# Performance work log

Measured on AMD Instinct MI355X. Metric: run time of the kernel, lower is better.

The kernel has to match this reference:

```python
import jax, jax.numpy as jnp
import numpy as np

U, I, D = 100000, 150000, 64
N = U + I
E = 1250000
KEEP_RATE = 0.8


def setup_inputs() -> dict:
    key = jax.random.key(0)
    k1, k2, k3, k4, k5, k6 = jax.random.split(key, 6)
    row = jax.random.randint(k1, (E,), 0, N, dtype=jnp.int32)
    col = jax.random.randint(k2, (E,), 0, N, dtype=jnp.int32)
    adj_values = jax.random.uniform(k3, (E,), dtype=jnp.float32)
    # edge dropout mask: floor(rand + keep_rate) in {0,1}, exactly as SpAdjEdgeDrop
    edge_mask = jnp.floor(jax.random.uniform(k4, (E,), dtype=jnp.float32) + KEEP_RATE)
    user_embeds = jax.random.normal(k5, (U, D), dtype=jnp.float32)
    item_embeds = jax.random.normal(k6, (I, D), dtype=jnp.float32)
    return {
        "row": row,
        "col": col,
        "adj_values": adj_values,
        "edge_mask": edge_mask,
        "user_embeds": user_embeds,
        "item_embeds": item_embeds,
        "layer_num": 3,
    }


def reference(row, col, adj_values, edge_mask, user_embeds, item_embeds, layer_num):
    user_num = user_embeds.shape[0]
    n_nodes = user_num + item_embeds.shape[0]
    # edge-dropped sparse values (mask==0 edges contribute nothing to spmm)
    vals = adj_values * edge_mask  # [E]
    embeds = jnp.concatenate([user_embeds, item_embeds], axis=0)  # [N, D]
    acc = embeds
    cur = embeds
    for _ in range(layer_num):
        # spmm: out[r] += vals[e] * cur[c] for each edge e=(r,c)
        msgs = vals[:, None] * cur[col]  # [E, D] gather
        cur = jax.ops.segment_sum(msgs, row, num_segments=n_nodes)  # [N, D] scatter-add
        acc = acc + cur
    out = acc / (layer_num + 1)
    return out[:user_num], out[user_num:]
```

## Files before the change

### kernel.cpp

```cpp
#include <hip/hip_runtime.h>


#define U_NODES 100000
#define N_NODES 250000
#define DIM4 16
#define E_EDGES 1250000
#define TILE_ROWS 1024
#define NT 245
#define NB 1024
#define GSZ (NB * 256)
#define BSEG 1280

typedef unsigned short u16;

__device__ __forceinline__ float bf2f(u16 h) {
    return __uint_as_float(((unsigned)h) << 16);
}
__device__ __forceinline__ u16 f2bf(float f) {
    unsigned u = __float_as_uint(f);
    u += 0x7fffu + ((u >> 16) & 1u);
    return (u16)(u >> 16);
}
__device__ __forceinline__ ushort4 gat(const u16* __restrict__ base, int node, int part) {
    return ((const ushort4*)(base + ((size_t)node << 6)))[part];
}
__device__ __forceinline__ void fma4(float4& s, float v, ushort4 h) {
    s.x += v * bf2f(h.x);
    s.y += v * bf2f(h.y);
    s.z += v * bf2f(h.z);
    s.w += v * bf2f(h.w);
}

__global__ void lgcn_part(const float4* __restrict__ user4,
                          const float4* __restrict__ item4,
                          u16* __restrict__ e0b,
                          const int* __restrict__ row,
                          const int* __restrict__ col,
                          const float* __restrict__ adj,
                          const float* __restrict__ mask,
                          int* __restrict__ OFF,
                          int2* __restrict__ staging) {
    __shared__ int lhist[256];
    __shared__ int lscan[256];
    __shared__ int loff[256];
    __shared__ int lcur[256];
    const int t = threadIdx.x;
    const int b = blockIdx.x;
    const int g0 = b * 256 + t;

    lhist[t] = 0;
    __syncthreads();

    for (int e = g0; e < E_EDGES; e += GSZ)
        if (mask[e] != 0.0f) atomicAdd(&lhist[row[e] >> 10], 1);
    __syncthreads();

    int v = lhist[t];
    lscan[t] = v;
    __syncthreads();
    for (int off = 1; off < 256; off <<= 1) {
        int u = (t >= off) ? lscan[t - off] : 0;
        __syncthreads();
        if (t >= off) lscan[t] += u;
        __syncthreads();
    }
    loff[t] = lscan[t] - v;
    lcur[t] = 0;
    __syncthreads();

    OFF[b * 256 + t] = loff[t];

    for (int e = g0; e < E_EDGES; e += GSZ) {
        float m = mask[e];
        if (m == 0.0f) continue;
        int r = row[e];
        int bkt = r >> 10;
        int rank = loff[bkt] + atomicAdd(&lcur[bkt], 1);
        staging[(size_t)b * BSEG + rank] =
            make_int2(((r & 1023) << 18) | col[e], __float_as_int(adj[e] * m));
    }

    const int CONV = N_NODES * 8;
    for (int i = g0; i < CONV; i += GSZ) {
        const int uc = U_NODES * 8;
        const float4* src = (i < uc) ? (user4 + 2 * (long)i)
                                     : (item4 + 2 * (long)(i - uc));
        float4 a = src[0];
        float4 bb = src[1];
        int4 o;
        o.x = (int)((unsigned)f2bf(a.x) | ((unsigned)f2bf(a.y) << 16));
        o.y = (int)((unsigned)f2bf(a.z) | ((unsigned)f2bf(a.w) << 16));
        o.z = (int)((unsigned)f2bf(bb.x) | ((unsigned)f2bf(bb.y) << 16));
        o.w = (int)((unsigned)f2bf(bb.z) | ((unsigned)f2bf(bb.w) << 16));
        ((int4*)e0b)[i] = o;
    }
}

__global__ void lgcn_build(const int* __restrict__ OFF,
                           const int2* __restrict__ staging,
                           int* __restrict__ total,
                           int2* __restrict__ rowdesc,
                           int2* __restrict__ csr) {
    __shared__ int S[NB];
    __shared__ int boff[NB];
    __shared__ int lcount[TILE_ROWS];
    __shared__ int lstart[TILE_ROWS];
    __shared__ int lcur[TILE_ROWS];
    __shared__ int lscan[256];
    __shared__ int sbase;
    const int i = blockIdx.x;
    const int t = threadIdx.x;

    int o0 = OFF[(4 * t + 0) * 256 + i], e0 = OFF[(4 * t + 0) * 256 + i + 1];
    int o1 = OFF[(4 * t + 1) * 256 + i], e1 = OFF[(4 * t + 1) * 256 + i + 1];
    int o2 = OFF[(4 * t + 2) * 256 + i], e2 = OFF[(4 * t + 2) * 256 + i + 1];
    int o3 = OFF[(4 * t + 3) * 256 + i], e3 = OFF[(4 * t + 3) * 256 + i + 1];
    int c0 = e0 - o0, c1 = e1 - o1, c2 = e2 - o2, c3 = e3 - o3;
    boff[4 * t + 0] = o0; boff[4 * t + 1] = o1;
    boff[4 * t + 2] = o2; boff[4 * t + 3] = o3;
    int sl = c0 + c1 + c2 + c3;
    lscan[t] = sl;
    __syncthreads();
    for (int off = 1; off < 256; off <<= 1) {
        int u = (t >= off) ? lscan[t - off] : 0;
        __syncthreads();
        if (t >= off) lscan[t] += u;
        __syncthreads();
    }
    int ex = lscan[t] - sl;
    S[4 * t + 0] = ex;
    S[4 * t + 1] = ex + c0;
    S[4 * t + 2] = ex + c0 + c1;
    S[4 * t + 3] = ex + c0 + c1 + c2;
    const int T = lscan[255];
    lcount[t] = 0; lcount[t + 256] = 0; lcount[t + 512] = 0; lcount[t + 768] = 0;
    __syncthreads();

    for (int j = t; j < T; j += 256) {
        int lo = 0, hi = NB;
        while (hi - lo > 1) { int mid = (lo + hi) >> 1; if (S[mid] <= j) lo = mid; else hi = mid; }
        int2 rec = staging[(size_t)lo * BSEG + boff[lo] + (j - S[lo])];
        atomicAdd(&lcount[((unsigned)rec.x) >> 18], 1);
    }
    __syncthreads();

    int d0 = lcount[4 * t + 0], d1 = lcount[4 * t + 1];
    int d2 = lcount[4 * t + 2], d3 = lcount[4 * t + 3];
    int p0 = (d0 + 3) & ~3, p1 = (d1 + 3) & ~3, p2 = (d2 + 3) & ~3, p3 = (d3 + 3) & ~3;
    int s = p0 + p1 + p2 + p3;
    __syncthreads();
    lscan[t] = s;
    __syncthreads();
    for (int off = 1; off < 256; off <<= 1) {
        int u = (t >= off) ? lscan[t - off] : 0;
        __syncthreads();
        if (t >= off) lscan[t] += u;
        __syncthreads();
    }
    if (t == 255) sbase = atomicAdd(total, lscan[255]);
    __syncthreads();
    const int tilesum = lscan[255];
    int pos = sbase + lscan[t] - s;
    int rbase = i * TILE_ROWS + 4 * t;
    if (rbase + 0 < N_NODES) rowdesc[rbase + 0] = make_int2(pos, d0);
    lstart[4 * t + 0] = pos; lcur[4 * t + 0] = 0; pos += p0;
    if (rbase + 1 < N_NODES) rowdesc[rbase + 1] = make_int2(pos, d1);
    lstart[4 * t + 1] = pos; lcur[4 * t + 1] = 0; pos += p1;
    if (rbase + 2 < N_NODES) rowdesc[rbase + 2] = make_int2(pos, d2);
    lstart[4 * t + 2] = pos; lcur[4 * t + 2] = 0; pos += p2;
    if (rbase + 3 < N_NODES) rowdesc[rbase + 3] = make_int2(pos, d3);
    lstart[4 * t + 3] = pos; lcur[4 * t + 3] = 0;
    __syncthreads();

    for (int j = t; j < tilesum; j += 256) csr[sbase + j] = make_int2(0, 0);
    __syncthreads();

    for (int j = t; j < T; j += 256) {
        int lo = 0, hi = NB;
        while (hi - lo > 1) { int mid = (lo + hi) >> 1; if (S[mid] <= j) lo = mid; else hi = mid; }
        int2 rec = staging[(size_t)lo * BSEG + boff[lo] + (j - S[lo])];
        int rw = ((unsigned)rec.x) >> 18;
        int rank = atomicAdd(&lcur[rw], 1);
        csr[lstart[rw] + rank] = make_int2(rec.x & 0x3FFFF, rec.y);
    }
}

template <bool LAST>
__global__ void lgcn_pull(const int2* __restrict__ rowdesc,
                          const int2* __restrict__ csr,
                          const u16*  __restrict__ curb,
                          const u16*  __restrict__ e0b,
                          const u16*  __restrict__ e1b,
                          u16*        __restrict__ outb,
                          float4*     __restrict__ out) {
    int tid = blockIdx.x * blockDim.x + threadIdx.x;
    int r = tid >> 4;
    int part = tid & 15;
    if (r >= N_NODES) return;
    int2 rd = rowdesc[r];
    int start = rd.x;
    int pend  = start + ((rd.y + 3) & ~3);
    float4 s = make_float4(0.f, 0.f, 0.f, 0.f);
    int e = start;
    for (; e + 8 <= pend; e += 8) {
        int4 ca = *(const int4*)(csr + e);
        int4 cb = *(const int4*)(csr + e + 2);
        int4 cc = *(const int4*)(csr + e + 4);
        int4 cd = *(const int4*)(csr + e + 6);
        ushort4 h0 = gat(curb, ca.x, part);
        ushort4 h1 = gat(curb, ca.z, part);
        ushort4 h2 = gat(curb, cb.x, part);
        ushort4 h3 = gat(curb, cb.z, part);
        ushort4 h4 = gat(curb, cc.x, part);
        ushort4 h5 = gat(curb, cc.z, part);
        ushort4 h6 = gat(curb, cd.x, part);
        ushort4 h7 = gat(curb, cd.z, part);
        fma4(s, __int_as_float(ca.y), h0);
        fma4(s, __int_as_float(ca.w), h1);
        fma4(s, __int_as_float(cb.y), h2);
        fma4(s, __int_as_float(cb.w), h3);
        fma4(s, __int_as_float(cc.y), h4);
        fma4(s, __int_as_float(cc.w), h5);
        fma4(s, __int_as_float(cd.y), h6);
        fma4(s, __int_as_float(cd.w), h7);
    }
    if (e < pend) {
        int4 ca = *(const int4*)(csr + e);
        int4 cb = *(const int4*)(csr + e + 2);
        ushort4 h0 = gat(curb, ca.x, part);
        ushort4 h1 = gat(curb, ca.z, part);
        ushort4 h2 = gat(curb, cb.x, part);
        ushort4 h3 = gat(curb, cb.z, part);
        fma4(s, __int_as_float(ca.y), h0);
        fma4(s, __int_as_float(ca.w), h1);
        fma4(s, __int_as_float(cb.y), h2);
        fma4(s, __int_as_float(cb.w), h3);
    }
    size_t oi = (size_t)r * DIM4 + part;
    if (LAST) {
        ushort4 a0 = ((const ushort4*)e0b)[oi];
        ushort4 a1 = ((const ushort4*)e1b)[oi];
        ushort4 a2 = ((const ushort4*)curb)[oi];
        out[oi] = make_float4(
            (s.x + bf2f(a0.x) + bf2f(a1.x) + bf2f(a2.x)) * 0.25f,
            (s.y + bf2f(a0.y) + bf2f(a1.y) + bf2f(a2.y)) * 0.25f,
            (s.z + bf2f(a0.z) + bf2f(a1.z) + bf2f(a2.z)) * 0.25f,
            (s.w + bf2f(a0.w) + bf2f(a1.w) + bf2f(a2.w)) * 0.25f);
    } else {
        ((ushort4*)outb)[oi] = make_ushort4(f2bf(s.x), f2bf(s.y), f2bf(s.z), f2bf(s.w));
    }
}

extern "C" void kernel_launch(void* const* d_in, const int* in_sizes, int n_in,
                              void* d_out, int out_size, void* d_ws, size_t ws_size,
                              hipStream_t stream) {
    const int*   row  = (const int*)d_in[0];
    const int*   col  = (const int*)d_in[1];
    const float* adj  = (const float*)d_in[2];
    const float* mask = (const float*)d_in[3];
    const float4* user4 = (const float4*)d_in[4];
    const float4* item4 = (const float4*)d_in[5];

    float4* acc = (float4*)d_out;

    const size_t bemb_bytes = (size_t)N_NODES * 64 * sizeof(u16);
    char* p = (char*)d_ws;
    u16* e0b = (u16*)p;  p += bemb_bytes;
    u16* e1b = (u16*)p;  p += bemb_bytes;
    u16* e2b = (u16*)p;  p += bemb_bytes;
    int* total = (int*)p;  p += 64;
    int* OFF   = (int*)p;  p += (size_t)NB * 256 * 4;
    int2* staging = (int2*)p;  p += (size_t)NB * BSEG * 8;
    int2* rowdesc = (int2*)p;  p += ((size_t)N_NODES * 8 + 63) & ~63ul;
    int2* csr     = (int2*)p;

    const int BLK = 256;
    const long node_vec4 = (long)N_NODES * DIM4;
    const int  grid_pull = (int)((node_vec4 + BLK - 1) / BLK);

    hipMemsetAsync(total, 0, 64, stream);
    lgcn_part<<<NB, BLK, 0, stream>>>(user4, item4, e0b, row, col, adj, mask,
                                      OFF, staging);
    lgcn_build<<<NT, BLK, 0, stream>>>(OFF, staging, total, rowdesc, csr);

    lgcn_pull<false><<<grid_pull, BLK, 0, stream>>>(rowdesc, csr, e0b, nullptr, nullptr, e1b, nullptr);
    lgcn_pull<false><<<grid_pull, BLK, 0, stream>>>(rowdesc, csr, e1b, nullptr, nullptr, e2b, nullptr);
    lgcn_pull<true ><<<grid_pull, BLK, 0, stream>>>(rowdesc, csr, e2b, e0b, e1b, nullptr, acc);
}
```

Before: 304.0 us.

## Split CSR build into count, scan, and place kernels with per-bucket parallelism

The single build kernel ran 245 blocks, each doing a binary search per edge to locate staging records. It is replaced by three kernels. Count and place use 4x more blocks; each thread walks one contiguous staging run directly with shared-memory atomics, and a separate scan kernel computes row offsets and per-group start positions. CSR zeroing moves to a hipMemsetAsync. This adds two launches, extra DEG/QSTART buffers and a larger memset over the whole CSR region, and edge order within a row may differ from before.

```diff
diff --git a/kernel.cpp b/kernel.cpp
--- a/kernel.cpp
+++ b/kernel.cpp
@@ -96,30 +96,47 @@
     }
 }
 
-__global__ void lgcn_build(const int* __restrict__ OFF,
+__global__ void lgcn_count(const int* __restrict__ OFF,
                            const int2* __restrict__ staging,
-                           int* __restrict__ total,
-                           int2* __restrict__ rowdesc,
-                           int2* __restrict__ csr) {
-    __shared__ int S[NB];
-    __shared__ int boff[NB];
+                           int* __restrict__ DEG) {
     __shared__ int lcount[TILE_ROWS];
-    __shared__ int lstart[TILE_ROWS];
-    __shared__ int lcur[TILE_ROWS];
+    const int i = blockIdx.x >> 2;
+    const int g = blockIdx.x & 3;
+    const int t = threadIdx.x;
+    lcount[t] = 0; lcount[t + 256] = 0; lcount[t + 512] = 0; lcount[t + 768] = 0;
+    __syncthreads();
+    const int b = (g << 8) + t;
+    const int o = OFF[(b << 8) + i];
+    const int n = OFF[(b << 8) + i + 1] - o;
+    const int2* run = staging + (size_t)b * BSEG + o;
+    for (int j = 0; j < n; ++j)
+        atomicAdd(&lcount[((unsigned)run[j].x) >> 18], 1);
+    __syncthreads();
+    const int base = ((i << 2) + g) << 10;
+    DEG[base + t]       = lcount[t];
+    DEG[base + t + 256] = lcount[t + 256];
+    DEG[base + t + 512] = lcount[t + 512];
+    DEG[base + t + 768] = lcount[t + 768];
+}
+
+__global__ void lgcn_scan(const int* __restrict__ DEG,
+                          int* __restrict__ total,
+                          int2* __restrict__ rowdesc,
+                          int* __restrict__ QSTART) {
     __shared__ int lscan[256];
     __shared__ int sbase;
     const int i = blockIdx.x;
     const int t = threadIdx.x;
-
-    int o0 = OFF[(4 * t + 0) * 256 + i], e0 = OFF[(4 * t + 0) * 256 + i + 1];
-    int o1 = OFF[(4 * t + 1) * 256 + i], e1 = OFF[(4 * t + 1) * 256 + i + 1];
-    int o2 = OFF[(4 * t + 2) * 256 + i], e2 = OFF[(4 * t + 2) * 256 + i + 1];
-    int o3 = OFF[(4 * t + 3) * 256 + i], e3 = OFF[(4 * t + 3) * 256 + i + 1];
-    int c0 = e0 - o0, c1 = e1 - o1, c2 = e2 - o2, c3 = e3 - o3;
-    boff[4 * t + 0] = o0; boff[4 * t + 1] = o1;
-    boff[4 * t + 2] = o2; boff[4 * t + 3] = o3;
-    int sl = c0 + c1 + c2 + c3;
-    lscan[t] = sl;
+    const int base = i << 12;
+
+    int a0 = DEG[base + 4*t+0], b0 = DEG[base+1024 + 4*t+0], c0 = DEG[base+2048 + 4*t+0], d0 = DEG[base+3072 + 4*t+0];
+    int a1 = DEG[base + 4*t+1], b1 = DEG[base+1024 + 4*t+1], c1 = DEG[base+2048 + 4*t+1], d1 = DEG[base+3072 + 4*t+1];
+    int a2 = DEG[base + 4*t+2], b2 = DEG[base+1024 + 4*t+2], c2 = DEG[base+2048 + 4*t+2], d2 = DEG[base+3072 + 4*t+2];
+    int a3 = DEG[base + 4*t+3], b3 = DEG[base+1024 + 4*t+3], c3 = DEG[base+2048 + 4*t+3], d3 = DEG[base+3072 + 4*t+3];
+    int deg0 = a0+b0+c0+d0, deg1 = a1+b1+c1+d1, deg2 = a2+b2+c2+d2, deg3 = a3+b3+c3+d3;
+    int p0 = (deg0+3)&~3, p1 = (deg1+3)&~3, p2 = (deg2+3)&~3, p3 = (deg3+3)&~3;
+    int s = p0 + p1 + p2 + p3;
+    lscan[t] = s;
     __syncthreads();
     for (int off = 1; off < 256; off <<= 1) {
         int u = (t >= off) ? lscan[t - off] : 0;
@@ -127,61 +144,60 @@
         if (t >= off) lscan[t] += u;
         __syncthreads();
     }
-    int ex = lscan[t] - sl;
-    S[4 * t + 0] = ex;
-    S[4 * t + 1] = ex + c0;
-    S[4 * t + 2] = ex + c0 + c1;
-    S[4 * t + 3] = ex + c0 + c1 + c2;
-    const int T = lscan[255];
-    lcount[t] = 0; lcount[t + 256] = 0; lcount[t + 512] = 0; lcount[t + 768] = 0;
-    __syncthreads();
-
-    for (int j = t; j < T; j += 256) {
-        int lo = 0, hi = NB;
-        while (hi - lo > 1) { int mid = (lo + hi) >> 1; if (S[mid] <= j) lo = mid; else hi = mid; }
-        int2 rec = staging[(size_t)lo * BSEG + boff[lo] + (j - S[lo])];
-        atomicAdd(&lcount[((unsigned)rec.x) >> 18], 1);
-    }
-    __syncthreads();
-
-    int d0 = lcount[4 * t + 0], d1 = lcount[4 * t + 1];
-    int d2 = lcount[4 * t + 2], d3 = lcount[4 * t + 3];
-    int p0 = (d0 + 3) & ~3, p1 = (d1 + 3) & ~3, p2 = (d2 + 3) & ~3, p3 = (d3 + 3) & ~3;
-    int s = p0 + p1 + p2 + p3;
-    __syncthreads();
-    lscan[t] = s;
-    __syncthreads();
-    for (int off = 1; off < 256; off <<= 1) {
-        int u = (t >= off) ? lscan[t - off] : 0;
-        __syncthreads();
-        if (t >= off) lscan[t] += u;
-        __syncthreads();
-    }
     if (t == 255) sbase = atomicAdd(total, lscan[255]);
     __syncthreads();
-    const int tilesum = lscan[255];
     int pos = sbase + lscan[t] - s;
-    int rbase = i * TILE_ROWS + 4 * t;
-    if (rbase + 0 < N_NODES) rowdesc[rbase + 0] = make_int2(pos, d0);
-    lstart[4 * t + 0] = pos; lcur[4 * t + 0] = 0; pos += p0;
-    if (rbase + 1 < N_NODES) rowdesc[rbase + 1] = make_int2(pos, d1);
-    lstart[4 * t + 1] = pos; lcur[4 * t + 1] = 0; pos += p1;
-    if (rbase + 2 < N_NODES) rowdesc[rbase + 2] = make_int2(pos, d2);
-    lstart[4 * t + 2] = pos; lcur[4 * t + 2] = 0; pos += p2;
-    if (rbase + 3 < N_NODES) rowdesc[rbase + 3] = make_int2(pos, d3);
-    lstart[4 * t + 3] = pos; lcur[4 * t + 3] = 0;
-    __syncthreads();
-
-    for (int j = t; j < tilesum; j += 256) csr[sbase + j] = make_int2(0, 0);
-    __syncthreads();
-
-    for (int j = t; j < T; j += 256) {
-        int lo = 0, hi = NB;
-        while (hi - lo > 1) { int mid = (lo + hi) >> 1; if (S[mid] <= j) lo = mid; else hi = mid; }
-        int2 rec = staging[(size_t)lo * BSEG + boff[lo] + (j - S[lo])];
+    const int rbase = (i << 10) + 4 * t;
+
+    int q = pos;
+    if (rbase + 0 < N_NODES) rowdesc[rbase + 0] = make_int2(pos, deg0);
+    QSTART[base + 4*t+0] = q; q += a0;
+    QSTART[base+1024 + 4*t+0] = q; q += b0;
+    QSTART[base+2048 + 4*t+0] = q; q += c0;
+    QSTART[base+3072 + 4*t+0] = q;
+    pos += p0; q = pos;
+    if (rbase + 1 < N_NODES) rowdesc[rbase + 1] = make_int2(pos, deg1);
+    QSTART[base + 4*t+1] = q; q += a1;
+    QSTART[base+1024 + 4*t+1] = q; q += b1;
+    QSTART[base+2048 + 4*t+1] = q; q += c1;
+    QSTART[base+3072 + 4*t+1] = q;
+    pos += p1; q = pos;
+    if (rbase + 2 < N_NODES) rowdesc[rbase + 2] = make_int2(pos, deg2);
+    QSTART[base + 4*t+2] = q; q += a2;
+    QSTART[base+1024 + 4*t+2] = q; q += b2;
+    QSTART[base+2048 + 4*t+2] = q; q += c2;
+    QSTART[base+3072 + 4*t+2] = q;
+    pos += p2; q = pos;
+    if (rbase + 3 < N_NODES) rowdesc[rbase + 3] = make_int2(pos, deg3);
+    QSTART[base + 4*t+3] = q; q += a3;
+    QSTART[base+1024 + 4*t+3] = q; q += b3;
+    QSTART[base+2048 + 4*t+3] = q; q += c3;
+    QSTART[base+3072 + 4*t+3] = q;
+}
+
+__global__ void lgcn_place(const int* __restrict__ OFF,
+                           const int2* __restrict__ staging,
+                           const int* __restrict__ QSTART,
+                           int2* __restrict__ csr) {
+    __shared__ int lcur[TILE_ROWS];
+    const int i = blockIdx.x >> 2;
+    const int g = blockIdx.x & 3;
+    const int t = threadIdx.x;
+    const int base = ((i << 2) + g) << 10;
+    lcur[t]       = QSTART[base + t];
+    lcur[t + 256] = QSTART[base + t + 256];
+    lcur[t + 512] = QSTART[base + t + 512];
+    lcur[t + 768] = QSTART[base + t + 768];
+    __syncthreads();
+    const int b = (g << 8) + t;
+    const int o = OFF[(b << 8) + i];
+    const int n = OFF[(b << 8) + i + 1] - o;
+    const int2* run = staging + (size_t)b * BSEG + o;
+    for (int j = 0; j < n; ++j) {
+        int2 rec = run[j];
         int rw = ((unsigned)rec.x) >> 18;
-        int rank = atomicAdd(&lcur[rw], 1);
-        csr[lstart[rw] + rank] = make_int2(rec.x & 0x3FFFF, rec.y);
+        int idx = atomicAdd(&lcur[rw], 1);
+        csr[idx] = make_int2(rec.x & 0x3FFFF, rec.y);
     }
 }
 
@@ -270,18 +286,24 @@
     u16* e2b = (u16*)p;  p += bemb_bytes;
     int* total = (int*)p;  p += 64;
     int* OFF   = (int*)p;  p += (size_t)NB * 256 * 4;
+    int* DEG   = (int*)p;  p += (size_t)NT * 4 * 1024 * 4;
+    int* QSTART= (int*)p;  p += (size_t)NT * 4 * 1024 * 4;
     int2* staging = (int2*)p;  p += (size_t)NB * BSEG * 8;
     int2* rowdesc = (int2*)p;  p += ((size_t)N_NODES * 8 + 63) & ~63ul;
     int2* csr     = (int2*)p;
+    const size_t csr_bytes = ((size_t)E_EDGES + 3 * N_NODES) * 8;
 
     const int BLK = 256;
     const long node_vec4 = (long)N_NODES * DIM4;
     const int  grid_pull = (int)((node_vec4 + BLK - 1) / BLK);
 
     hipMemsetAsync(total, 0, 64, stream);
+    hipMemsetAsync(csr, 0, csr_bytes, stream);
     lgcn_part<<<NB, BLK, 0, stream>>>(user4, item4, e0b, row, col, adj, mask,
                                       OFF, staging);
-    lgcn_build<<<NT, BLK, 0, stream>>>(OFF, staging, total, rowdesc, csr);
+    lgcn_count<<<NT * 4, BLK, 0, stream>>>(OFF, staging, DEG);
+    lgcn_scan<<<NT, BLK, 0, stream>>>(DEG, total, rowdesc, QSTART);
+    lgcn_place<<<NT * 4, BLK, 0, stream>>>(OFF, staging, QSTART, csr);
 
     lgcn_pull<false><<<grid_pull, BLK, 0, stream>>>(rowdesc, csr, e0b, nullptr, nullptr, e1b, nullptr);
     lgcn_pull<false><<<grid_pull, BLK, 0, stream>>>(rowdesc, csr, e1b, nullptr, nullptr, e2b, nullptr);
```

New measurement: 299.7 us. About the same (-1.4%).

## Cache edge rows in registers, walk staging runs directly, use fixed per-tile CSR slots

Applied to the files above, without the earlier changes.

The partition kernel now keeps each thread's five edges' row and mask in registers, so the scatter pass does not reload row and mask. The scatter also moves after the bf16 conversion loop, which may help hide the first pass's latency. The build kernel drops the per-element binary search over source blocks: each thread walks its four contiguous staging runs sequentially. The global atomic tile offset is replaced by a fixed per-tile capacity (TCAP=8192), and zeroing CSR padding becomes one memset. This assumes at most five edges per thread and at most 8192 padded edges per tile, and the sequential per-thread runs may be poorly balanced and uncoalesced.

```diff
diff --git a/kernel.cpp b/kernel.cpp
--- a/kernel.cpp
+++ b/kernel.cpp
@@ -10,6 +10,7 @@
 #define NB 1024
 #define GSZ (NB * 256)
 #define BSEG 1280
+#define TCAP 8192
 
 typedef unsigned short u16;
 
@@ -51,8 +52,20 @@
     lhist[t] = 0;
     __syncthreads();
 
-    for (int e = g0; e < E_EDGES; e += GSZ)
-        if (mask[e] != 0.0f) atomicAdd(&lhist[row[e] >> 10], 1);
+    int r0 = -1, r1 = -1, r2 = -1, r3 = -1, r4 = -1;
+    float v0 = 0.f, v1 = 0.f, v2 = 0.f, v3 = 0.f, v4 = 0.f;
+    {
+        int e = g0;
+        if (e < E_EDGES) { float m = mask[e]; if (m != 0.f) { r0 = row[e]; v0 = m; atomicAdd(&lhist[r0 >> 10], 1); } }
+        e += GSZ;
+        if (e < E_EDGES) { float m = mask[e]; if (m != 0.f) { r1 = row[e]; v1 = m; atomicAdd(&lhist[r1 >> 10], 1); } }
+        e += GSZ;
+        if (e < E_EDGES) { float m = mask[e]; if (m != 0.f) { r2 = row[e]; v2 = m; atomicAdd(&lhist[r2 >> 10], 1); } }
+        e += GSZ;
+        if (e < E_EDGES) { float m = mask[e]; if (m != 0.f) { r3 = row[e]; v3 = m; atomicAdd(&lhist[r3 >> 10], 1); } }
+        e += GSZ;
+        if (e < E_EDGES) { float m = mask[e]; if (m != 0.f) { r4 = row[e]; v4 = m; atomicAdd(&lhist[r4 >> 10], 1); } }
+    }
     __syncthreads();
 
     int v = lhist[t];
@@ -69,16 +82,6 @@
     __syncthreads();
 
     OFF[b * 256 + t] = loff[t];
-
-    for (int e = g0; e < E_EDGES; e += GSZ) {
-        float m = mask[e];
-        if (m == 0.0f) continue;
-        int r = row[e];
-        int bkt = r >> 10;
-        int rank = loff[bkt] + atomicAdd(&lcur[bkt], 1);
-        staging[(size_t)b * BSEG + rank] =
-            make_int2(((r & 1023) << 18) | col[e], __float_as_int(adj[e] * m));
-    }
 
     const int CONV = N_NODES * 8;
     for (int i = g0; i < CONV; i += GSZ) {
@@ -94,61 +97,61 @@
         o.w = (int)((unsigned)f2bf(bb.z) | ((unsigned)f2bf(bb.w) << 16));
         ((int4*)e0b)[i] = o;
     }
+    __syncthreads();
+
+    {
+        int e = g0;
+        if (r0 >= 0) { int bkt = r0 >> 10; int rank = loff[bkt] + atomicAdd(&lcur[bkt], 1);
+            staging[(size_t)b * BSEG + rank] = make_int2(((r0 & 1023) << 18) | col[e], __float_as_int(adj[e] * v0)); }
+        e += GSZ;
+        if (r1 >= 0) { int bkt = r1 >> 10; int rank = loff[bkt] + atomicAdd(&lcur[bkt], 1);
+            staging[(size_t)b * BSEG + rank] = make_int2(((r1 & 1023) << 18) | col[e], __float_as_int(adj[e] * v1)); }
+        e += GSZ;
+        if (r2 >= 0) { int bkt = r2 >> 10; int rank = loff[bkt] + atomicAdd(&lcur[bkt], 1);
+            staging[(size_t)b * BSEG + rank] = make_int2(((r2 & 1023) << 18) | col[e], __float_as_int(adj[e] * v2)); }
+        e += GSZ;
+        if (r3 >= 0) { int bkt = r3 >> 10; int rank = loff[bkt] + atomicAdd(&lcur[bkt], 1);
+            staging[(size_t)b * BSEG + rank] = make_int2(((r3 & 1023) << 18) | col[e], __float_as_int(adj[e] * v3)); }
+        e += GSZ;
+        if (r4 >= 0) { int bkt = r4 >> 10; int rank = loff[bkt] + atomicAdd(&lcur[bkt], 1);
+            staging[(size_t)b * BSEG + rank] = make_int2(((r4 & 1023) << 18) | col[e], __float_as_int(adj[e] * v4)); }
+    }
 }
 
 __global__ void lgcn_build(const int* __restrict__ OFF,
                            const int2* __restrict__ staging,
-                           int* __restrict__ total,
                            int2* __restrict__ rowdesc,
                            int2* __restrict__ csr) {
-    __shared__ int S[NB];
-    __shared__ int boff[NB];
     __shared__ int lcount[TILE_ROWS];
     __shared__ int lstart[TILE_ROWS];
     __shared__ int lcur[TILE_ROWS];
     __shared__ int lscan[256];
-    __shared__ int sbase;
     const int i = blockIdx.x;
     const int t = threadIdx.x;
 
-    int o0 = OFF[(4 * t + 0) * 256 + i], e0 = OFF[(4 * t + 0) * 256 + i + 1];
-    int o1 = OFF[(4 * t + 1) * 256 + i], e1 = OFF[(4 * t + 1) * 256 + i + 1];
-    int o2 = OFF[(4 * t + 2) * 256 + i], e2 = OFF[(4 * t + 2) * 256 + i + 1];
-    int o3 = OFF[(4 * t + 3) * 256 + i], e3 = OFF[(4 * t + 3) * 256 + i + 1];
-    int c0 = e0 - o0, c1 = e1 - o1, c2 = e2 - o2, c3 = e3 - o3;
-    boff[4 * t + 0] = o0; boff[4 * t + 1] = o1;
-    boff[4 * t + 2] = o2; boff[4 * t + 3] = o3;
-    int sl = c0 + c1 + c2 + c3;
-    lscan[t] = sl;
-    __syncthreads();
-    for (int off = 1; off < 256; off <<= 1) {
-        int u = (t >= off) ? lscan[t - off] : 0;
-        __syncthreads();
-        if (t >= off) lscan[t] += u;
-        __syncthreads();
-    }
-    int ex = lscan[t] - sl;
-    S[4 * t + 0] = ex;
-    S[4 * t + 1] = ex + c0;
-    S[4 * t + 2] = ex + c0 + c1;
-    S[4 * t + 3] = ex + c0 + c1 + c2;
-    const int T = lscan[255];
     lcount[t] = 0; lcount[t + 256] = 0; lcount[t + 512] = 0; lcount[t + 768] = 0;
     __syncthreads();
 
-    for (int j = t; j < T; j += 256) {
-        int lo = 0, hi = NB;
-        while (hi - lo > 1) { int mid = (lo + hi) >> 1; if (S[mid] <= j) lo = mid; else hi = mid; }
-        int2 rec = staging[(size_t)lo * BSEG + boff[lo] + (j - S[lo])];
-        atomicAdd(&lcount[((unsigned)rec.x) >> 18], 1);
-    }
+    const int b0 = t, b1 = t + 256, b2 = t + 512, b3 = t + 768;
+    const int o0 = OFF[(b0 << 8) + i], n0 = OFF[(b0 << 8) + i + 1] - o0;
+    const int o1 = OFF[(b1 << 8) + i], n1 = OFF[(b1 << 8) + i + 1] - o1;
+    const int o2 = OFF[(b2 << 8) + i], n2 = OFF[(b2 << 8) + i + 1] - o2;
+    const int o3 = OFF[(b3 << 8) + i], n3 = OFF[(b3 << 8) + i + 1] - o3;
+    const int2* run0 = staging + (size_t)b0 * BSEG + o0;
+    const int2* run1 = staging + (size_t)b1 * BSEG + o1;
+    const int2* run2 = staging + (size_t)b2 * BSEG + o2;
+    const int2* run3 = staging + (size_t)b3 * BSEG + o3;
+
+    for (int j = 0; j < n0; ++j) atomicAdd(&lcount[((unsigned)run0[j].x) >> 18], 1);
+    for (int j = 0; j < n1; ++j) atomicAdd(&lcount[((unsigned)run1[j].x) >> 18], 1);
+    for (int j = 0; j < n2; ++j) atomicAdd(&lcount[((unsigned)run2[j].x) >> 18], 1);
+    for (int j = 0; j < n3; ++j) atomicAdd(&lcount[((unsigned)run3[j].x) >> 18], 1);
     __syncthreads();
 
     int d0 = lcount[4 * t + 0], d1 = lcount[4 * t + 1];
     int d2 = lcount[4 * t + 2], d3 = lcount[4 * t + 3];
     int p0 = (d0 + 3) & ~3, p1 = (d1 + 3) & ~3, p2 = (d2 + 3) & ~3, p3 = (d3 + 3) & ~3;
     int s = p0 + p1 + p2 + p3;
-    __syncthreads();
     lscan[t] = s;
     __syncthreads();
     for (int off = 1; off < 256; off <<= 1) {
@@ -157,32 +160,26 @@
         if (t >= off) lscan[t] += u;
         __syncthreads();
     }
-    if (t == 255) sbase = atomicAdd(total, lscan[255]);
-    __syncthreads();
-    const int tilesum = lscan[255];
-    int pos = sbase + lscan[t] - s;
-    int rbase = i * TILE_ROWS + 4 * t;
+    int pos = i * TCAP + lscan[t] - s;
+    const int rbase = (i << 10) + 4 * t;
     if (rbase + 0 < N_NODES) rowdesc[rbase + 0] = make_int2(pos, d0);
-    lstart[4 * t + 0] = pos; lcur[4 * t + 0] = 0; pos += p0;
+    lstart[4 * t + 0] = pos; lcur[4 * t + 0] = pos; pos += p0;
     if (rbase + 1 < N_NODES) rowdesc[rbase + 1] = make_int2(pos, d1);
-    lstart[4 * t + 1] = pos; lcur[4 * t + 1] = 0; pos += p1;
+    lstart[4 * t + 1] = pos; lcur[4 * t + 1] = pos; pos += p1;
     if (rbase + 2 < N_NODES) rowdesc[rbase + 2] = make_int2(pos, d2);
-    lstart[4 * t + 2] = pos; lcur[4 * t + 2] = 0; pos += p2;
+    lstart[4 * t + 2] = pos; lcur[4 * t + 2] = pos; pos += p2;
     if (rbase + 3 < N_NODES) rowdesc[rbase + 3] = make_int2(pos, d3);
-    lstart[4 * t + 3] = pos; lcur[4 * t + 3] = 0;
-    __syncthreads();
-
-    for (int j = t; j < tilesum; j += 256) csr[sbase + j] = make_int2(0, 0);
-    __syncthreads();
-
-    for (int j = t; j < T; j += 256) {
-        int lo = 0, hi = NB;
-        while (hi - lo > 1) { int mid = (lo + hi) >> 1; if (S[mid] <= j) lo = mid; else hi = mid; }
-        int2 rec = staging[(size_t)lo * BSEG + boff[lo] + (j - S[lo])];
-        int rw = ((unsigned)rec.x) >> 18;
-        int rank = atomicAdd(&lcur[rw], 1);
-        csr[lstart[rw] + rank] = make_int2(rec.x & 0x3FFFF, rec.y);
-    }
+    lstart[4 * t + 3] = pos; lcur[4 * t + 3] = pos;
+    __syncthreads();
+
+    for (int j = 0; j < n0; ++j) { int2 rec = run0[j]; int rw = ((unsigned)rec.x) >> 18;
+        csr[atomicAdd(&lcur[rw], 1)] = make_int2(rec.x & 0x3FFFF, rec.y); }
+    for (int j = 0; j < n1; ++j) { int2 rec = run1[j]; int rw = ((unsigned)rec.x) >> 18;
+        csr[atomicAdd(&lcur[rw], 1)] = make_int2(rec.x & 0x3FFFF, rec.y); }
+    for (int j = 0; j < n2; ++j) { int2 rec = run2[j]; int rw = ((unsigned)rec.x) >> 18;
+        csr[atomicAdd(&lcur[rw], 1)] = make_int2(rec.x & 0x3FFFF, rec.y); }
+    for (int j = 0; j < n3; ++j) { int2 rec = run3[j]; int rw = ((unsigned)rec.x) >> 18;
+        csr[atomicAdd(&lcur[rw], 1)] = make_int2(rec.x & 0x3FFFF, rec.y); }
 }
 
 template <bool LAST>
@@ -268,20 +265,20 @@
     u16* e0b = (u16*)p;  p += bemb_bytes;
     u16* e1b = (u16*)p;  p += bemb_bytes;
     u16* e2b = (u16*)p;  p += bemb_bytes;
-    int* total = (int*)p;  p += 64;
     int* OFF   = (int*)p;  p += (size_t)NB * 256 * 4;
     int2* staging = (int2*)p;  p += (size_t)NB * BSEG * 8;
     int2* rowdesc = (int2*)p;  p += ((size_t)N_NODES * 8 + 63) & ~63ul;
     int2* csr     = (int2*)p;
+    const size_t csr_bytes = (size_t)NT * TCAP * 8;
 
     const int BLK = 256;
     const long node_vec4 = (long)N_NODES * DIM4;
     const int  grid_pull = (int)((node_vec4 + BLK - 1) / BLK);
 
-    hipMemsetAsync(total, 0, 64, stream);
+    hipMemsetAsync(csr, 0, csr_bytes, stream);
     lgcn_part<<<NB, BLK, 0, stream>>>(user4, item4, e0b, row, col, adj, mask,
                                       OFF, staging);
-    lgcn_build<<<NT, BLK, 0, stream>>>(OFF, staging, total, rowdesc, csr);
+    lgcn_build<<<NT, BLK, 0, stream>>>(OFF, staging, rowdesc, csr);
 
     lgcn_pull<false><<<grid_pull, BLK, 0, stream>>>(rowdesc, csr, e0b, nullptr, nullptr, e1b, nullptr);
     lgcn_pull<false><<<grid_pull, BLK, 0, stream>>>(rowdesc, csr, e1b, nullptr, nullptr, e2b, nullptr);
```

Result: faster. 297.3 us (-2.2%).
